# Kernel tuning notes

Hardware: AMD Instinct MI355X
Metric: run time of the kernel (lower is better)

Reference implementation:

```python
import jax, jax.numpy as jnp
import numpy as np

B, S, DIM, H, G, DH = 1, 2048, 2048, 16, 2, 128
L, D, LP, NSEL, W = 32, 16, 32, 16, 256   # compress len, stride, select block, top-k blocks, window
REP = H // G


def setup_inputs() -> dict:
    key = jax.random.key(0)
    ks = jax.random.split(key, 8)
    x = jax.random.normal(ks[0], (B, S, DIM), jnp.float32)
    inv = 1.0 / (10000.0 ** (jnp.arange(0, DH, 2, dtype=jnp.float32) / DH))
    ang = jnp.outer(jnp.arange(S, dtype=jnp.float32), inv)   # [S, DH//2]
    freqs_cos, freqs_sin = jnp.cos(ang), jnp.sin(ang)
    std = 0.02
    wq = jax.random.normal(ks[1], (DIM, H * DH), jnp.float32) * std
    wk = jax.random.normal(ks[2], (DIM, G * DH), jnp.float32) * std
    wv = jax.random.normal(ks[3], (DIM, G * DH), jnp.float32) * std
    wo = jax.random.normal(ks[4], (H * DH, DIM), jnp.float32) * std
    w_g = jax.random.normal(ks[5], (DH, 3), jnp.float32) * std
    return dict(x=x, freqs_cos=freqs_cos, freqs_sin=freqs_sin,
                wq=wq, wk=wk, wv=wv, wo=wo, w_g=w_g, start_pos=0)


def _rope(t, cos, sin):
    # t: [B,S,heads,DH]; complex pairs are consecutive elements (view_as_complex semantics)
    x0, x1 = t[..., 0::2], t[..., 1::2]
    c, s = cos[None, :, None, :], sin[None, :, None, :]
    return jnp.stack([x0 * c - x1 * s, x0 * s + x1 * c], axis=-1).reshape(t.shape)


def _nsa_forward(x, freqs_cos, freqs_sin, wq, wk, wv, wo, w_g):
    scale = DH ** -0.5
    q = (x @ wq).reshape(B, S, H, DH)
    k = (x @ wk).reshape(B, S, G, DH)
    v = (x @ wv).reshape(B, S, G, DH)
    q = _rope(q, freqs_cos, freqs_sin).reshape(B, S, G, REP, DH)
    k = _rope(k, freqs_cos, freqs_sin)

    tpos = jnp.arange(S)
    NEG = jnp.float32(-1e30)

    # ---- branch 1: compressed-block attention ----
    J = (S - L) // D + 1
    starts = jnp.arange(J) * D
    blk_idx = starts[:, None] + jnp.arange(L)[None, :]            # [J, L]
    k_cmp = k[:, blk_idx].mean(axis=2)                            # [B,J,G,DH]
    v_cmp = v[:, blk_idx].mean(axis=2)
    s_cmp = jnp.einsum('bsgrd,bjgd->bsgrj', q, k_cmp) * scale
    valid = (starts[None, :] + L - 1) <= tpos[:, None]            # [S, J]
    p_cmp = jax.nn.softmax(jnp.where(valid[None, :, None, None, :], s_cmp, NEG), axis=-1)
    p_cmp = jnp.where(valid.any(-1)[None, :, None, None, None], p_cmp, 0.0)
    o_cmp = jnp.einsum('bsgrj,bjgd->bsgrd', p_cmp, v_cmp)

    # ---- branch 2: top-n selected-block attention ----
    NB = S // LP
    sel_start = jnp.arange(NB) * LP
    # overlap of cmp block [j*D, j*D+L) with selection block [m*LP, m*LP+LP)
    ov = (starts[:, None] < sel_start[None, :] + LP) & (starts[:, None] + L > sel_start[None, :])
    imp = jnp.einsum('bsgrj,jm->bsgm', p_cmp, ov.astype(jnp.float32))   # sum over heads in group
    blk_causal = sel_start[None, :] <= tpos[:, None]                    # [S, NB]
    imp = jnp.where(blk_causal[None, :, None, :], imp, -jnp.inf)
    cur_blk = tpos // LP
    force = jax.nn.one_hot(cur_blk, NB) + jax.nn.one_hot(jnp.zeros_like(cur_blk), NB)
    imp = imp + force[None, :, None, :] * 1e9                           # always keep init + current block
    _, top_idx = jax.lax.top_k(imp, NSEL)                               # [B,S,G,NSEL]
    blk_mask = jax.nn.one_hot(top_idx, NB).sum(axis=-2) > 0             # [B,S,G,NB]
    tok_sel = jnp.repeat(blk_mask, LP, axis=-1)                         # [B,S,G,S]
    causal = tpos[:, None] >= tpos[None, :]                             # [S,S]

    s_full = jnp.einsum('bsgrd,btgd->bsgrt', q, k) * scale              # [B,S,G,R,S]
    m_sel = tok_sel[:, :, :, None, :] & causal[None, :, None, None, :]
    p_sel = jax.nn.softmax(jnp.where(m_sel, s_full, NEG), axis=-1)
    o_sel = jnp.einsum('bsgrt,btgd->bsgrd', p_sel, v)

    # ---- branch 3: sliding-window attention ----
    m_sw = causal & (tpos[None, :] > tpos[:, None] - W)
    p_sw = jax.nn.softmax(jnp.where(m_sw[None, :, None, None, :], s_full, NEG), axis=-1)
    o_sw = jnp.einsum('bsgrt,btgd->bsgrd', p_sw, v)

    # ---- learned gated combination ----
    g = jax.nn.sigmoid(jnp.einsum('bsgrd,de->bsgre', q, w_g))
    out = g[..., 0:1] * o_cmp + g[..., 1:2] * o_sel + g[..., 2:3] * o_sw
    return out.reshape(B, S, H * DH) @ wo


def reference(x, freqs_cos, freqs_sin, wq, wk, wv, wo, w_g, start_pos):
    return _nsa_forward(x, freqs_cos, freqs_sin, wq, wk, wv, wo, w_g)
```

## Files before the change

kernel.cpp:

```cpp
#include <hip/hip_runtime.h>
#include <cstddef>
#include <cstdint>
#include <math.h>

#define kS    2048
#define kDim  2048
#define kH    16
#define kG    2
#define kDH   128
#define kRep  8
#define kL    32
#define kDstr 16
#define kLP   32
#define kNSel 16
#define kW    256
#define kJ    127
#define kNB   64
#define kScale 0.08838834764831845f
#define kQT   4
#define kQF   8
#define kLDQ  2560

#define kKP   136
#define kVP   40

typedef __attribute__((ext_vector_type(4))) float f32x4;
typedef __attribute__((ext_vector_type(8))) __bf16 bf16x8;
typedef __attribute__((ext_vector_type(4))) __bf16 bf16x4;

__device__ __forceinline__ unsigned short f2bf(float f) {
  unsigned u = __float_as_uint(f);
  u += 0x7fff + ((u >> 16) & 1);
  return (unsigned short)(u >> 16);
}

#define GLDS16(src, dst)                                                     \
  __builtin_amdgcn_global_load_lds(                                          \
      (const __attribute__((address_space(1))) unsigned int*)(src),          \
      (__attribute__((address_space(3))) unsigned int*)(dst), 16, 0, 0)

__global__ void cast_bf16_kernel(const float* __restrict__ in,
                                 unsigned short* __restrict__ out, int n4) {
  int i = blockIdx.x * blockDim.x + threadIdx.x;
  if (i >= n4) return;
  float4 v = reinterpret_cast<const float4*>(in)[i];
  ushort4 o;
  o.x = f2bf(v.x); o.y = f2bf(v.y); o.z = f2bf(v.z); o.w = f2bf(v.w);
  reinterpret_cast<ushort4*>(out)[i] = o;
}

__global__ __launch_bounds__(256) void transpose_cast_kernel(
    const float* __restrict__ in, int ldin, unsigned short* __restrict__ out,
    int rows, int cols) {
  __shared__ float tile[32][33];
  const int bx = blockIdx.x * 32;
  const int by = blockIdx.y * 32;
  const int tx = threadIdx.x & 31;
  const int ty = threadIdx.x >> 5;
#pragma unroll
  for (int i = 0; i < 32; i += 8)
    tile[ty + i][tx] = in[(size_t)(by + ty + i) * ldin + bx + tx];
  __syncthreads();
#pragma unroll
  for (int i = 0; i < 32; i += 8)
    out[(size_t)(bx + ty + i) * rows + by + tx] = f2bf(tile[tx][ty + i]);
}

__global__ __launch_bounds__(512) void gemm_bf16_kernel(
    const unsigned short* __restrict__ A,
    const unsigned short* __restrict__ Bt,
    float* __restrict__ C, int M, int N, int ldc, int K) {
  __shared__ __align__(16) unsigned short As[128 * 32];
  __shared__ __align__(16) unsigned short Bs[128 * 32];
  const int t = threadIdx.x;
  const int lane = t & 63;
  const int wid = t >> 6;
  const int wr = wid >> 2;
  const int wc = wid & 3;
  const int lhi = lane >> 4, llo = lane & 15;
  const size_t row0 = (size_t)blockIdx.y * 128;
  const size_t col0 = (size_t)blockIdx.x * 128;

  f32x4 acc[4][2];
#pragma unroll
  for (int m = 0; m < 4; ++m)
#pragma unroll
    for (int n = 0; n < 2; ++n) acc[m][n] = f32x4{0.f, 0.f, 0.f, 0.f};

  const int e0 = t * 8;
  const int r0 = e0 >> 5, kk0 = e0 & 31;

  for (int k0 = 0; k0 < K; k0 += 32) {
    GLDS16(A + (row0 + r0) * (size_t)K + k0 + kk0, As + e0);
    GLDS16(Bt + (col0 + r0) * (size_t)K + k0 + kk0, Bs + e0);
    __syncthreads();
    bf16x8 af[4], bfr[2];
#pragma unroll
    for (int m = 0; m < 4; ++m)
      af[m] = *reinterpret_cast<const bf16x8*>(&As[(wr * 64 + m * 16 + llo) * 32 + lhi * 8]);
#pragma unroll
    for (int n = 0; n < 2; ++n)
      bfr[n] = *reinterpret_cast<const bf16x8*>(&Bs[(wc * 32 + n * 16 + llo) * 32 + lhi * 8]);
#pragma unroll
    for (int m = 0; m < 4; ++m)
#pragma unroll
      for (int n = 0; n < 2; ++n)
        acc[m][n] = __builtin_amdgcn_mfma_f32_16x16x32_bf16(af[m], bfr[n], acc[m][n], 0, 0, 0);
    __syncthreads();
  }
#pragma unroll
  for (int m = 0; m < 4; ++m)
#pragma unroll
    for (int n = 0; n < 2; ++n)
#pragma unroll
      for (int j = 0; j < 4; ++j) {
        size_t r = row0 + wr * 64 + m * 16 + lhi * 4 + j;
        size_t c = col0 + wc * 32 + n * 16 + llo;
        C[r * (size_t)ldc + c] = acc[m][n][j];
      }
}

__global__ void rope_kernel(float* __restrict__ tb, int ld,
                            const float* __restrict__ fc,
                            const float* __restrict__ fsn, int nheads, int total,
                            unsigned short* __restrict__ outb, int ldout) {
  int idx = blockIdx.x * blockDim.x + threadIdx.x;
  if (idx >= total) return;
  int i = idx & 63;
  int h = (idx >> 6) % nheads;
  int s = idx / (64 * nheads);
  float c = fc[s * 64 + i];
  float sn = fsn[s * 64 + i];
  float* p = tb + (size_t)s * ld + h * kDH + 2 * i;
  float x0 = p[0], x1 = p[1];
  float r0 = x0 * c - x1 * sn;
  float r1 = x0 * sn + x1 * c;
  p[0] = r0;
  p[1] = r1;
  unsigned short* o = outb + (size_t)s * ldout + h * kDH + 2 * i;
  o[0] = f2bf(r0);
  o[1] = f2bf(r1);
}

__global__ void pool_kernel(const float* __restrict__ qkv,
                            float* __restrict__ kcT,
                            unsigned short* __restrict__ vcT) {
  int idx = blockIdx.x * blockDim.x + threadIdx.x;
  if (idx >= 128 * kG * kDH) return;
  int d = idx & 127;
  int g = (idx >> 7) & 1;
  int j = idx >> 8;
  float sk = 0.f, sv = 0.f;
  if (j < kJ) {
    for (int l = 0; l < kL; ++l) {
      size_t row = (size_t)(j * kDstr + l) * kLDQ;
      sk += qkv[row + kDim + g * kDH + d];
      sv += qkv[row + kDim + kG * kDH + g * kDH + d];
    }
    sk *= (1.f / 32.f);
    sv *= (1.f / 32.f);
  }
  size_t o = ((size_t)(g * 128 + d)) * 128 + j;
  kcT[o] = sk;
  vcT[o] = f2bf(sv);
}

__global__ __launch_bounds__(256) void cmp_attn_kernel(
    const float* __restrict__ qkv, const float* __restrict__ kcT,
    const unsigned short* __restrict__ vcT,
    const float* __restrict__ wg,
    float* __restrict__ oc, float* __restrict__ gates,
    unsigned long long* __restrict__ selmask) {
  __shared__ float qst[128][36];
  __shared__ float pT [128][36];
  __shared__ __align__(16) char ubuf[32 * 132 * 4];
  float (*kvt)[132] = reinterpret_cast<float(*)[132]>(ubuf);
  unsigned short (*pTb)[136] = reinterpret_cast<unsigned short(*)[136]>(ubuf);

  const int b = blockIdx.x;
  const int g = b & 1;
  const int s0 = (b >> 1) * kQT;
  const int t = threadIdx.x;
  const int ty = t >> 5;
  const int tx = t & 31;

  {
    int row = t & 31;
    int dl = (t >> 5) * 16;
    const float* src = qkv + (size_t)(s0 + (row >> 3)) * kLDQ +
                       (g * kRep + (row & 7)) * kDH + dl;
#pragma unroll
    for (int i = 0; i < 4; ++i) {
      float4 v = *reinterpret_cast<const float4*>(src + i * 4);
      qst[dl + i * 4 + 0][row] = v.x;
      qst[dl + i * 4 + 1][row] = v.y;
      qst[dl + i * 4 + 2][row] = v.z;
      qst[dl + i * 4 + 3][row] = v.w;
    }
  }
  __syncthreads();

  float S[4][4];
#pragma unroll
  for (int rr = 0; rr < 4; ++rr)
#pragma unroll
    for (int jj = 0; jj < 4; ++jj) S[rr][jj] = 0.f;

  for (int dt = 0; dt < 4; ++dt) {
    {
      const float* base = kcT + (size_t)(g * 128 + dt * 32) * 128;
#pragma unroll
      for (int i = 0; i < 4; ++i) {
        int s = t + i * 256;
        int dd = s >> 5;
        int j4 = s & 31;
        *reinterpret_cast<float4*>(&kvt[dd][j4 * 4]) =
            *reinterpret_cast<const float4*>(base + dd * 128 + j4 * 4);
      }
    }
    __syncthreads();
#pragma unroll
    for (int kk = 0; kk < 32; ++kk) {
      float4 a = *reinterpret_cast<const float4*>(&qst[dt * 32 + kk][ty * 4]);
      float4 bb = *reinterpret_cast<const float4*>(&kvt[kk][tx * 4]);
      float av[4] = {a.x, a.y, a.z, a.w};
      float bv[4] = {bb.x, bb.y, bb.z, bb.w};
#pragma unroll
      for (int rr = 0; rr < 4; ++rr)
#pragma unroll
        for (int jj = 0; jj < 4; ++jj)
          S[rr][jj] = fmaf(av[rr], bv[jj], S[rr][jj]);
    }
    __syncthreads();
  }

#pragma unroll
  for (int rr = 0; rr < 4; ++rr) {
    int row = ty * 4 + rr;
    int s = s0 + (row >> 3);
    int jmax = (s >= kL - 1) ? ((s - (kL - 1)) >> 4) : -1;
#pragma unroll
    for (int jj = 0; jj < 4; ++jj) {
      int j = tx * 4 + jj;
      pT[j][row] = (j <= jmax && j < kJ) ? S[rr][jj] * kScale : -1e30f;
    }
  }
  __syncthreads();

  {
    int row = t >> 3;
    int l = t & 7;
    int s = s0 + (row >> 3);
    if (s < kL - 1) {
#pragma unroll
      for (int i = 0; i < 16; ++i) pT[l + i * 8][row] = 0.f;
    } else {
      float vals[16];
      float mx = -INFINITY;
#pragma unroll
      for (int i = 0; i < 16; ++i) {
        vals[i] = pT[l + i * 8][row];
        mx = fmaxf(mx, vals[i]);
      }
      mx = fmaxf(mx, __shfl_xor(mx, 1));
      mx = fmaxf(mx, __shfl_xor(mx, 2));
      mx = fmaxf(mx, __shfl_xor(mx, 4));
      float sm = 0.f;
#pragma unroll
      for (int i = 0; i < 16; ++i) {
        vals[i] = __expf(vals[i] - mx);
        sm += vals[i];
      }
      sm += __shfl_xor(sm, 1);
      sm += __shfl_xor(sm, 2);
      sm += __shfl_xor(sm, 4);
      float inv = 1.f / sm;
#pragma unroll
      for (int i = 0; i < 16; ++i) pT[l + i * 8][row] = vals[i] * inv;
    }
  }
  __syncthreads();

  {
    int row = t >> 3;
    int l = t & 7;
#pragma unroll
    for (int i = 0; i < 16; ++i)
      pTb[row][l + i * 8] = f2bf(pT[l + i * 8][row]);
  }
  {
    int qq = t >> 6;
    int m = t & 63;
    int s = s0 + qq;
    int mcur = s >> 5;
    float im;
    if (m > mcur) {
      im = -INFINITY;
    } else {
      im = 0.f;
#pragma unroll
      for (int r = 0; r < 8; ++r) {
        int row = qq * 8 + r;
        float sp = (2 * m - 1 >= 0) ? pT[2 * m - 1][row] : 0.f;
        sp += pT[2 * m][row];
        if (2 * m + 1 < kJ) sp += pT[2 * m + 1][row];
        im += sp;
      }
      if (m == 0) im += 1e9f;
      if (m == mcur) im += 1e9f;
    }
    bool taken = false;
    unsigned long long mask = 0ull;
    for (int it = 0; it < kNSel; ++it) {
      float cv = taken ? -INFINITY : im;
      int ci = taken ? 64 : m;
#pragma unroll
      for (int off = 1; off < 64; off <<= 1) {
        float ov = __shfl_xor(cv, off);
        int oi = __shfl_xor(ci, off);
        if (ov > cv || (ov == cv && oi < ci)) { cv = ov; ci = oi; }
      }
      mask |= 1ull << ci;
      if (m == ci) taken = true;
    }
    if (m == 0) selmask[(size_t)s * 2 + g] = mask;
  }
  if (t < 192) {
    int task = t >> 1;
    int p = t & 1;
    int row = task / 3;
    int e = task - row * 3;
    int sQ = s0 + (row >> 3);
    int r = row & 7;
    const float* qr = qkv + (size_t)sQ * kLDQ + (g * kRep + r) * kDH + p * 64;
    float acc = 0.f;
#pragma unroll
    for (int i = 0; i < 16; ++i) {
      float4 v = *reinterpret_cast<const float4*>(qr + i * 4);
      int d = p * 64 + i * 4;
      acc = fmaf(v.x, wg[d * 3 + e], acc);
      acc = fmaf(v.y, wg[(d + 1) * 3 + e], acc);
      acc = fmaf(v.z, wg[(d + 2) * 3 + e], acc);
      acc = fmaf(v.w, wg[(d + 3) * 3 + e], acc);
    }
    acc += __shfl_xor(acc, 1);
    if (p == 0)
      gates[((size_t)(sQ * 2 + g) * kRep + r) * 3 + e] = 1.f / (1.f + __expf(-acc));
  }
  __syncthreads();

  {
    const int lane = t & 63;
    const int wv = t >> 6;
    const int lo = lane & 15, hi = lane >> 4;
    f32x4 acc[2][2];
#pragma unroll
    for (int rt = 0; rt < 2; ++rt)
#pragma unroll
      for (int dt2 = 0; dt2 < 2; ++dt2) acc[rt][dt2] = f32x4{0.f, 0.f, 0.f, 0.f};
#pragma unroll
    for (int ks = 0; ks < 4; ++ks) {
      bf16x8 pf[2], vf[2];
#pragma unroll
      for (int rt = 0; rt < 2; ++rt)
        pf[rt] = *reinterpret_cast<const bf16x8*>(&pTb[rt * 16 + lo][ks * 32 + hi * 8]);
#pragma unroll
      for (int dt2 = 0; dt2 < 2; ++dt2)
        vf[dt2] = *reinterpret_cast<const bf16x8*>(
            vcT + ((size_t)(g * 128 + wv * 32 + dt2 * 16 + lo)) * 128 + ks * 32 + hi * 8);
#pragma unroll
      for (int rt = 0; rt < 2; ++rt)
#pragma unroll
        for (int dt2 = 0; dt2 < 2; ++dt2)
          acc[rt][dt2] = __builtin_amdgcn_mfma_f32_16x16x32_bf16(vf[dt2], pf[rt], acc[rt][dt2], 0, 0, 0);
    }
#pragma unroll
    for (int rt = 0; rt < 2; ++rt) {
      int qrow = rt * 16 + lo;
      size_t base = ((size_t)(s0 + (qrow >> 3)) * kH + g * kRep + (qrow & 7)) * kDH;
#pragma unroll
      for (int dt2 = 0; dt2 < 2; ++dt2) {
        int d0 = wv * 32 + dt2 * 16 + hi * 4;
#pragma unroll
        for (int jj = 0; jj < 4; ++jj)
          oc[base + d0 + jj] = acc[rt][dt2][jj];
      }
    }
  }
}

template <int MODE>
__device__ __forceinline__ void attn_tile3(
    const unsigned short* __restrict__ Ksb, const unsigned short* __restrict__ VTb,
    const bf16x8 (&qf)[4], __bf16* Psw,
    int tb, unsigned selw, int wv, int lo, int hi, int s0,
    f32x4 (&O)[8], float& mst, float& lst) {
  f32x4 S0 = f32x4{0.f, 0.f, 0.f, 0.f};
  f32x4 S1 = f32x4{0.f, 0.f, 0.f, 0.f};
  __builtin_amdgcn_s_setprio(1);
#pragma unroll
  for (int ds = 0; ds < 4; ++ds) {
    bf16x8 a0 = *reinterpret_cast<const bf16x8*>(&Ksb[lo * kKP + ds * 32 + hi * 8]);
    bf16x8 a1 = *reinterpret_cast<const bf16x8*>(&Ksb[(16 + lo) * kKP + ds * 32 + hi * 8]);
    S0 = __builtin_amdgcn_mfma_f32_16x16x32_bf16(a0, qf[ds], S0, 0, 0, 0);
    S1 = __builtin_amdgcn_mfma_f32_16x16x32_bf16(a1, qf[ds], S1, 0, 0, 0);
  }
  __builtin_amdgcn_s_setprio(0);
  const int qloc = wv * 2 + (lo >> 3);
  const int s_row = s0 + qloc;
  const bool selq = (MODE == 1) || (((selw >> qloc) & 1u) != 0);
  float sv[2][4];
#pragma unroll
  for (int j = 0; j < 4; ++j) { sv[0][j] = S0[j]; sv[1][j] = S1[j]; }
#pragma unroll
  for (int tf = 0; tf < 2; ++tf)
#pragma unroll
    for (int j = 0; j < 4; ++j) {
      int tok = tb + tf * 16 + hi * 4 + j;
      bool ok = selq && (tok <= s_row) && (MODE == 0 || tok > s_row - kW);
      sv[tf][j] = ok ? sv[tf][j] * kScale : -1e30f;
    }
  float pm = sv[0][0];
#pragma unroll
  for (int tf = 0; tf < 2; ++tf)
#pragma unroll
    for (int j = 0; j < 4; ++j) pm = fmaxf(pm, sv[tf][j]);
  pm = fmaxf(pm, __shfl_xor(pm, 16));
  pm = fmaxf(pm, __shfl_xor(pm, 32));
  if (__any(pm > mst + 8.f)) {
    float mn = fmaxf(mst, pm);
    float f = __expf(mst - mn);
#pragma unroll
    for (int df = 0; df < 8; ++df)
#pragma unroll
      for (int j = 0; j < 4; ++j) O[df][j] *= f;
    lst *= f;
    mst = mn;
  }
  float lacc = 0.f;
#pragma unroll
  for (int tf = 0; tf < 2; ++tf) {
    bf16x4 pk;
#pragma unroll
    for (int j = 0; j < 4; ++j) {
      float e = __expf(sv[tf][j] - mst);
      lacc += e;
      pk[j] = (__bf16)e;
    }
    *reinterpret_cast<bf16x4*>(&Psw[lo * 40 + tf * 16 + hi * 4]) = pk;
  }
  lst += lacc;
  bf16x8 pfrag = *reinterpret_cast<const bf16x8*>(&Psw[lo * 40 + hi * 8]);
  __builtin_amdgcn_s_setprio(1);
#pragma unroll
  for (int df = 0; df < 8; ++df) {
    bf16x8 vf = *reinterpret_cast<const bf16x8*>(&VTb[(df * 16 + lo) * kVP + hi * 8]);
    O[df] = __builtin_amdgcn_mfma_f32_16x16x32_bf16(vf, pfrag, O[df], 0, 0, 0);
  }
  __builtin_amdgcn_s_setprio(0);
}

__global__ __launch_bounds__(256) void fused_attn_kernel(
    const unsigned short* __restrict__ qb, const unsigned short* __restrict__ kb,
    const unsigned short* __restrict__ vT, const float* __restrict__ ocp,
    const float* __restrict__ gts,
    const unsigned long long* __restrict__ selmask,
    unsigned short* __restrict__ preb) {
  __shared__ __align__(16) unsigned short Ks[2][32 * kKP];
  __shared__ __align__(16) unsigned short VTs[2][128 * kVP];
  __shared__ __align__(16) __bf16 Ps[4][16 * 40];
  __shared__ unsigned long long qm[kQF];
  __shared__ unsigned char selbits[kNB];
  __shared__ unsigned char blist[kNB];
  __shared__ int nsel_sh;

  const int bid = blockIdx.x;
  const int g = bid & 1;
  const int idx = bid >> 1;
  const int qt = (idx < 128) ? idx : 383 - idx;
  const int s0 = qt * kQF;
  const int t = threadIdx.x;
  const int lane = t & 63;
  const int wv = t >> 6;
  const int lo = lane & 15, hi = lane >> 4;

  int kBase[3], vBase[3];
#pragma unroll
  for (int ii = 0; ii < 3; ++ii) {
    int s = t + ii * 256;
    int r = s / 17, c = s - r * 17;
    if (c > 15) c = 0;
    kBase[ii] = r * 256 + g * 128 + c * 8;
    int r2 = s / 5, c2 = s - r2 * 5;
    if (c2 > 3) c2 = 0;
    vBase[ii] = (g * 128 + r2) * 2048 + c2 * 8;
  }
  auto STAGE = [&](int tb, unsigned short* Ksb, unsigned short* VTb) {
#pragma unroll
    for (int ii = 0; ii < 3; ++ii) {
      if (ii < 2 || t < 32)
        GLDS16(kb + (size_t)tb * 256 + kBase[ii], Ksb + (t + ii * 256) * 8);
      if (ii < 2 || t < 128)
        GLDS16(vT + (size_t)vBase[ii] + tb, VTb + (t + ii * 256) * 8);
    }
  };

  const int qrow = wv * 16 + lo;
  const int s_q = s0 + (qrow >> 3);
  const int hd = qrow & 7;
  bf16x8 qf[4];
  {
    const unsigned short* src = qb + ((size_t)s_q * 16 + g * 8 + hd) * 128 + hi * 8;
#pragma unroll
    for (int ds = 0; ds < 4; ++ds)
      qf[ds] = *reinterpret_cast<const bf16x8*>(src + ds * 32);
  }
  if (t < kQF) {
    int sQ = s0 + t;
    unsigned long long mm = selmask[(size_t)sQ * 2 + g];
    mm &= ((2ull << (sQ >> 5)) - 1ull);
    qm[t] = mm;
  }
  __syncthreads();
  if (t < kNB) {
    unsigned b = 0;
    for (int ql = 0; ql < kQF; ++ql)
      b |= (unsigned)((qm[ql] >> t) & 1ull) << ql;
    selbits[t] = (unsigned char)b;
  }
  if (t == 0) {
    unsigned long long u = 0;
    for (int ql = 0; ql < kQF; ++ql) u |= qm[ql];
    int n = 0;
    for (int m = 0; m < kNB; ++m)
      if ((u >> m) & 1ull) blist[n++] = (unsigned char)m;
    nsel_sh = n;
  }
  __syncthreads();

  __bf16* Psw = &Ps[wv][0];

  f32x4 O1[8], O2[8];
#pragma unroll
  for (int df = 0; df < 8; ++df) O1[df] = f32x4{0.f, 0.f, 0.f, 0.f};
  float mst = -INFINITY, lst = 0.f;

  const int nsel = nsel_sh;
  int cur = 0;
  STAGE((int)blist[0] * 32, Ks[0], VTs[0]);
  __syncthreads();
  for (int i = 0; i < nsel; ++i) {
    if (i + 1 < nsel)
      STAGE((int)blist[i + 1] * 32, Ks[cur ^ 1], VTs[cur ^ 1]);
    int b = blist[i];
    attn_tile3<0>(Ks[cur], VTs[cur], qf, Psw, b * 32, selbits[b], wv, lo, hi, s0,
                  O1, mst, lst);
    __syncthreads();
    cur ^= 1;
  }
  const int hi_t = s0 >> 5;
  const int lo_t = (s0 > 255) ? ((s0 - 255) >> 5) : 0;
  STAGE(hi_t * 32, Ks[cur], VTs[cur]);
  float g0v, g2v;
  {
    const float* gp = gts + ((size_t)(s_q * 2 + g) * 8 + hd) * 3;
    g0v = gp[0];
    g2v = gp[2];
    float lt = lst;
    lt += __shfl_xor(lt, 16);
    lt += __shfl_xor(lt, 32);
    float f = gp[1] / lt;
#pragma unroll
    for (int df = 0; df < 8; ++df)
#pragma unroll
      for (int j = 0; j < 4; ++j) O1[df][j] *= f;
  }
  mst = -INFINITY;
  lst = 0.f;
#pragma unroll
  for (int df = 0; df < 8; ++df) O2[df] = f32x4{0.f, 0.f, 0.f, 0.f};
  __syncthreads();

  for (int tt = hi_t; tt >= lo_t; --tt) {
    if (tt - 1 >= lo_t)
      STAGE((tt - 1) * 32, Ks[cur ^ 1], VTs[cur ^ 1]);
    attn_tile3<1>(Ks[cur], VTs[cur], qf, Psw, tt * 32, 0u, wv, lo, hi, s0,
                  O2, mst, lst);
    __syncthreads();
    cur ^= 1;
  }

  {
    float lt = lst;
    lt += __shfl_xor(lt, 16);
    lt += __shfl_xor(lt, 32);
    float f2 = g2v / lt;
    size_t base = ((size_t)s_q * 16 + g * 8 + hd) * 128;
#pragma unroll
    for (int df = 0; df < 8; ++df) {
      int d0 = df * 16 + hi * 4;
      float4 ocv = *reinterpret_cast<const float4*>(&ocp[base + d0]);
      ushort4 w;
      w.x = f2bf(g0v * ocv.x + O1[df][0] + f2 * O2[df][0]);
      w.y = f2bf(g0v * ocv.y + O1[df][1] + f2 * O2[df][1]);
      w.z = f2bf(g0v * ocv.z + O1[df][2] + f2 * O2[df][2]);
      w.w = f2bf(g0v * ocv.w + O1[df][3] + f2 * O2[df][3]);
      *reinterpret_cast<ushort4*>(&preb[base + d0]) = w;
    }
  }
}

extern "C" void kernel_launch(void* const* d_in, const int* in_sizes, int n_in,
                              void* d_out, int out_size, void* d_ws, size_t ws_size,
                              hipStream_t stream) {
  (void)in_sizes; (void)n_in; (void)out_size; (void)ws_size;
  const float* x  = (const float*)d_in[0];
  const float* fc = (const float*)d_in[1];
  const float* fs = (const float*)d_in[2];
  const float* wq = (const float*)d_in[3];
  const float* wk = (const float*)d_in[4];
  const float* wv = (const float*)d_in[5];
  const float* wo = (const float*)d_in[6];
  const float* wg = (const float*)d_in[7];
  float* out = (float*)d_out;

  float* qkv  = (float*)d_ws;
  float* kcT  = qkv + (size_t)kS * kLDQ;
  float* oc   = kcT + 256 * 128;
  float* gts  = oc + kS * kH * kDH;
  unsigned long long* selmask = (unsigned long long*)(gts + kS * kG * kRep * 3);
  unsigned short* xb   = (unsigned short*)(selmask + kS * kG);
  unsigned short* wqT  = xb + kS * kDim;
  unsigned short* wkT  = wqT + (kH * kDH) * kDim;
  unsigned short* wvT  = wkT + (kG * kDH) * kDim;
  unsigned short* woT  = wvT + (kG * kDH) * kDim;
  unsigned short* preb = woT + kDim * (kH * kDH);
  unsigned short* kb   = preb + kS * kDim;
  unsigned short* vT   = kb + kS * kG * kDH;
  unsigned short* vcTb = vT + kS * kG * kDH;
  unsigned short* qbuf = xb;

  dim3 blk256(256);
  dim3 blk512(512);
  cast_bf16_kernel<<<kS * kDim / 4 / 256, blk256, 0, stream>>>(x, xb, kS * kDim / 4);
  transpose_cast_kernel<<<dim3((kH * kDH) / 32, kDim / 32), blk256, 0, stream>>>(wq, kH * kDH, wqT, kDim, kH * kDH);
  transpose_cast_kernel<<<dim3((kG * kDH) / 32, kDim / 32), blk256, 0, stream>>>(wk, kG * kDH, wkT, kDim, kG * kDH);
  transpose_cast_kernel<<<dim3((kG * kDH) / 32, kDim / 32), blk256, 0, stream>>>(wv, kG * kDH, wvT, kDim, kG * kDH);
  transpose_cast_kernel<<<dim3(kDim / 32, (kH * kDH) / 32), blk256, 0, stream>>>(wo, kDim, woT, kH * kDH, kDim);
  gemm_bf16_kernel<<<dim3(kLDQ / 128, kS / 128), blk512, 0, stream>>>(
      xb, wqT, qkv, kS, kLDQ, kLDQ, kDim);
  rope_kernel<<<8192, blk256, 0, stream>>>(qkv, kLDQ, fc, fs, kH, kS * kH * 64, qbuf, kDim);
  rope_kernel<<<1024, blk256, 0, stream>>>(qkv + kDim, kLDQ, fc, fs, kG, kS * kG * 64, kb, kG * kDH);
  transpose_cast_kernel<<<dim3(kG * kDH / 32, kS / 32), blk256, 0, stream>>>(
      qkv + kDim + kG * kDH, kLDQ, vT, kS, kG * kDH);
  pool_kernel<<<128, blk256, 0, stream>>>(qkv, kcT, vcTb);
  cmp_attn_kernel<<<kS / kQT * kG, blk256, 0, stream>>>(qkv, kcT, vcTb, wg, oc, gts, selmask);
  fused_attn_kernel<<<kS / kQF * kG, blk256, 0, stream>>>(qbuf, kb, vT, oc, gts, selmask, preb);
  gemm_bf16_kernel<<<dim3(kDim / 128, kS / 128), blk512, 0, stream>>>(
      preb, woT, out, kS, kDim, kDim, kH * kDH);
}
```

Baseline: 266.2 us.

## Merge selected and window tile loops into one triple-buffered pipeline

The fused attention kernel now builds a single tile list covering the selected blocks followed by the sliding-window tiles, and runs one loop over it. K and V are staged into a unified triple-buffered LDS region with a prefetch distance of two tiles, and completion is tracked with explicit vmcnt waits plus a raw barrier instead of __syncthreads. This removes the pipeline drain and refill between the two branches and hides more load latency. In exchange it uses more LDS per block, which could reduce occupancy, and it relies on hand-tuned vmcnt counts that must match the five loads issued per stage.

```diff
diff --git a/kernel.cpp b/kernel.cpp
--- a/kernel.cpp
+++ b/kernel.cpp
@@ -23,6 +23,7 @@
 
 #define kKP   136
 #define kVP   40
+#define kNSlot 1280
 
 typedef __attribute__((ext_vector_type(4))) float f32x4;
 typedef __attribute__((ext_vector_type(8))) __bf16 bf16x8;
@@ -466,13 +467,12 @@
     const float* __restrict__ gts,
     const unsigned long long* __restrict__ selmask,
     unsigned short* __restrict__ preb) {
-  __shared__ __align__(16) unsigned short Ks[2][32 * kKP];
-  __shared__ __align__(16) unsigned short VTs[2][128 * kVP];
+  __shared__ __align__(16) unsigned short KV[3][kNSlot * 8];
   __shared__ __align__(16) __bf16 Ps[4][16 * 40];
   __shared__ unsigned long long qm[kQF];
   __shared__ unsigned char selbits[kNB];
-  __shared__ unsigned char blist[kNB];
-  __shared__ int nsel_sh;
+  __shared__ unsigned char tlist[kNB + 12];
+  __shared__ int nsel_sh, ntiles_sh;
 
   const int bid = blockIdx.x;
   const int g = bid & 1;
@@ -484,36 +484,46 @@
   const int wv = t >> 6;
   const int lo = lane & 15, hi = lane >> 4;
 
-  int kBase[3], vBase[3];
-#pragma unroll
-  for (int ii = 0; ii < 3; ++ii) {
-    int s = t + ii * 256;
-    int r = s / 17, c = s - r * 17;
-    if (c > 15) c = 0;
-    kBase[ii] = r * 256 + g * 128 + c * 8;
-    int r2 = s / 5, c2 = s - r2 * 5;
-    if (c2 > 3) c2 = 0;
-    vBase[ii] = (g * 128 + r2) * 2048 + c2 * 8;
-  }
-  auto STAGE = [&](int tb, unsigned short* Ksb, unsigned short* VTb) {
-#pragma unroll
-    for (int ii = 0; ii < 3; ++ii) {
-      if (ii < 2 || t < 32)
-        GLDS16(kb + (size_t)tb * 256 + kBase[ii], Ksb + (t + ii * 256) * 8);
-      if (ii < 2 || t < 128)
-        GLDS16(vT + (size_t)vBase[ii] + tb, VTb + (t + ii * 256) * 8);
-    }
+  const unsigned short* bp[5];
+  int mult[5];
+#pragma unroll
+  for (int j = 0; j < 5; ++j) {
+    int s = t + j * 256;
+    if (s < 544) {
+      int r = s / 17, c = s - r * 17;
+      if (c > 15) c = 0;
+      bp[j] = kb + r * 256 + g * 128 + c * 8;
+      mult[j] = 256;
+    } else if (s < 1184) {
+      int v = s - 544;
+      int r2 = v / 5, c2 = v - r2 * 5;
+      if (c2 > 3) c2 = 0;
+      bp[j] = vT + (size_t)(g * 128 + r2) * 2048 + c2 * 8;
+      mult[j] = 1;
+    } else {
+      bp[j] = kb + g * 128;
+      mult[j] = 256;
+    }
+  }
+  auto STAGE = [&](int tb, int bi) {
+    unsigned short* dst = &KV[bi][(size_t)t * 8];
+#pragma unroll
+    for (int j = 0; j < 5; ++j)
+      GLDS16(bp[j] + (size_t)tb * mult[j], dst + j * 2048);
   };
 
   const int qrow = wv * 16 + lo;
   const int s_q = s0 + (qrow >> 3);
   const int hd = qrow & 7;
   bf16x8 qf[4];
+  float g0v, g1v, g2v;
   {
     const unsigned short* src = qb + ((size_t)s_q * 16 + g * 8 + hd) * 128 + hi * 8;
 #pragma unroll
     for (int ds = 0; ds < 4; ++ds)
       qf[ds] = *reinterpret_cast<const bf16x8*>(src + ds * 32);
+    const float* gp = gts + ((size_t)(s_q * 2 + g) * 8 + hd) * 3;
+    g0v = gp[0]; g1v = gp[1]; g2v = gp[2];
   }
   if (t < kQF) {
     int sQ = s0 + t;
@@ -533,61 +543,67 @@
     for (int ql = 0; ql < kQF; ++ql) u |= qm[ql];
     int n = 0;
     for (int m = 0; m < kNB; ++m)
-      if ((u >> m) & 1ull) blist[n++] = (unsigned char)m;
+      if ((u >> m) & 1ull) tlist[n++] = (unsigned char)m;
     nsel_sh = n;
+    int hi_t = s0 >> 5;
+    int lo_t = (s0 > 255) ? ((s0 - 255) >> 5) : 0;
+    for (int tt = hi_t; tt >= lo_t; --tt) tlist[n++] = (unsigned char)tt;
+    ntiles_sh = n;
   }
   __syncthreads();
 
   __bf16* Psw = &Ps[wv][0];
+  const int nsel = nsel_sh;
+  const int NT = ntiles_sh;
 
   f32x4 O1[8], O2[8];
 #pragma unroll
-  for (int df = 0; df < 8; ++df) O1[df] = f32x4{0.f, 0.f, 0.f, 0.f};
+  for (int df = 0; df < 8; ++df) {
+    O1[df] = f32x4{0.f, 0.f, 0.f, 0.f};
+    O2[df] = f32x4{0.f, 0.f, 0.f, 0.f};
+  }
   float mst = -INFINITY, lst = 0.f;
 
-  const int nsel = nsel_sh;
-  int cur = 0;
-  STAGE((int)blist[0] * 32, Ks[0], VTs[0]);
-  __syncthreads();
-  for (int i = 0; i < nsel; ++i) {
-    if (i + 1 < nsel)
-      STAGE((int)blist[i + 1] * 32, Ks[cur ^ 1], VTs[cur ^ 1]);
-    int b = blist[i];
-    attn_tile3<0>(Ks[cur], VTs[cur], qf, Psw, b * 32, selbits[b], wv, lo, hi, s0,
-                  O1, mst, lst);
-    __syncthreads();
-    cur ^= 1;
-  }
-  const int hi_t = s0 >> 5;
-  const int lo_t = (s0 > 255) ? ((s0 - 255) >> 5) : 0;
-  STAGE(hi_t * 32, Ks[cur], VTs[cur]);
-  float g0v, g2v;
-  {
-    const float* gp = gts + ((size_t)(s_q * 2 + g) * 8 + hd) * 3;
-    g0v = gp[0];
-    g2v = gp[2];
-    float lt = lst;
-    lt += __shfl_xor(lt, 16);
-    lt += __shfl_xor(lt, 32);
-    float f = gp[1] / lt;
-#pragma unroll
-    for (int df = 0; df < 8; ++df)
-#pragma unroll
-      for (int j = 0; j < 4; ++j) O1[df][j] *= f;
-  }
-  mst = -INFINITY;
-  lst = 0.f;
-#pragma unroll
-  for (int df = 0; df < 8; ++df) O2[df] = f32x4{0.f, 0.f, 0.f, 0.f};
-  __syncthreads();
-
-  for (int tt = hi_t; tt >= lo_t; --tt) {
-    if (tt - 1 >= lo_t)
-      STAGE((tt - 1) * 32, Ks[cur ^ 1], VTs[cur ^ 1]);
-    attn_tile3<1>(Ks[cur], VTs[cur], qf, Psw, tt * 32, 0u, wv, lo, hi, s0,
-                  O2, mst, lst);
-    __syncthreads();
-    cur ^= 1;
+  STAGE((int)tlist[0] * 32, 0);
+  STAGE((int)tlist[1] * 32, 1);
+  asm volatile("s_waitcnt vmcnt(5)" ::: "memory");
+  __builtin_amdgcn_s_barrier();
+  __builtin_amdgcn_sched_barrier(0);
+
+  for (int i = 0; i < NT; ++i) {
+    const int bufc = i % 3;
+    if (i + 2 < NT)
+      STAGE((int)tlist[i + 2] * 32, (i + 2) % 3);
+    const unsigned short* Ksb = &KV[bufc][0];
+    const unsigned short* VTb = &KV[bufc][544 * 8];
+    if (i < nsel) {
+      int b = tlist[i];
+      attn_tile3<0>(Ksb, VTb, qf, Psw, b * 32, selbits[b], wv, lo, hi, s0,
+                    O1, mst, lst);
+      if (i == nsel - 1) {
+        float lt = lst;
+        lt += __shfl_xor(lt, 16);
+        lt += __shfl_xor(lt, 32);
+        float f = g1v / lt;
+#pragma unroll
+        for (int df = 0; df < 8; ++df)
+#pragma unroll
+          for (int j = 0; j < 4; ++j) O1[df][j] *= f;
+        mst = -INFINITY;
+        lst = 0.f;
+      }
+    } else {
+      int tt = tlist[i];
+      attn_tile3<1>(Ksb, VTb, qf, Psw, tt * 32, 0u, wv, lo, hi, s0,
+                    O2, mst, lst);
+    }
+    if (i + 2 < NT) {
+      asm volatile("s_waitcnt vmcnt(5)" ::: "memory");
+    } else {
+      asm volatile("s_waitcnt vmcnt(0)" ::: "memory");
+    }
+    __builtin_amdgcn_s_barrier();
+    __builtin_amdgcn_sched_barrier(0);
   }
 
   {
```

New measurement: 282.6 us. 1.06x slower.
